# Kernel optimization log

Hardware: AMD Instinct MI355X
Metric: run time of the kernel (lower is better)

Reference implementation:

```python
import jax, jax.numpy as jnp
import numpy as np

NUM_WIRES = 14
N_LAYERS = 2
BATCH = 256
DIM = 2 ** NUM_WIRES


def setup_inputs() -> dict:
    key = jax.random.key(0)
    k1, k2, k3 = jax.random.split(key, 3)
    s = jax.random.normal(k1, (BATCH, DIM), dtype=jnp.float32)
    # StatePrep requires normalized amplitudes
    s = s / jnp.linalg.norm(s, axis=1, keepdims=True)
    params = jax.random.normal(k2, (N_LAYERS, NUM_WIRES, 3), dtype=jnp.float32)
    head_w = jax.random.normal(k3, (1, NUM_WIRES), dtype=jnp.float32) / np.sqrt(NUM_WIRES)
    head_b = jnp.zeros((1,), dtype=jnp.float32)
    return {"state_batch": s, "params": params, "head_w": head_w, "head_b": head_b}


def _ry(t):
    c = jnp.cos(t / 2).astype(jnp.complex64)
    s = jnp.sin(t / 2).astype(jnp.complex64)
    return jnp.stack([jnp.stack([c, -s]), jnp.stack([s, c])])


def _rz(t):
    tc = t.astype(jnp.complex64)
    e_m = jnp.exp(-0.5j * tc)
    e_p = jnp.exp(0.5j * tc)
    z = jnp.zeros((), jnp.complex64)
    return jnp.stack([jnp.stack([e_m, z]), jnp.stack([z, e_p])])


def _rx(t):
    c = jnp.cos(t / 2).astype(jnp.complex64)
    s = (-1j) * jnp.sin(t / 2).astype(jnp.complex64)
    return jnp.stack([jnp.stack([c, s]), jnp.stack([s, c])])


def _apply_1q(psi, U, wire):
    # psi: (B, 2, 2, ..., 2); contract 2x2 gate on axis wire+1 across the batch
    out = jnp.tensordot(U, psi, axes=([1], [wire + 1]))
    return jnp.moveaxis(out, 0, wire + 1)


def _apply_cnot(psi, control, target):
    # flip target axis where control bit == 1
    shape = [1] * psi.ndim
    shape[control + 1] = 2
    mask = (jnp.arange(2) == 1).reshape(shape)
    return jnp.where(mask, jnp.flip(psi, axis=target + 1), psi)


def _circuit(state_c, params):
    psi = state_c.reshape((BATCH,) + (2,) * NUM_WIRES)
    for layer in range(N_LAYERS):
        for w in range(NUM_WIRES):
            psi = _apply_1q(psi, _ry(params[layer, w, 0]), w)
            psi = _apply_1q(psi, _rz(params[layer, w, 1]), w)
            psi = _apply_cnot(psi, w, (w + 1) % NUM_WIRES)
            psi = _apply_1q(psi, _rx(params[layer, w, 2]), w)
    probs = (psi.real ** 2 + psi.imag ** 2).reshape(BATCH, DIM)
    # <Z_w> = sum over basis states of prob * (+1/-1 depending on bit of wire w)
    basis = jnp.arange(DIM)
    shifts = NUM_WIRES - 1 - jnp.arange(NUM_WIRES)  # wire 0 is the MSB axis
    signs = 1.0 - 2.0 * ((basis[None, :] >> shifts[:, None]) & 1).astype(jnp.float32)
    return probs @ signs.T  # (B, NUM_WIRES)


def reference(state_batch, params, head_w, head_b):
    feats = _circuit(state_batch.astype(jnp.complex64), params)  # (B, NUM_WIRES)
    return feats @ head_w[0] + head_b[0]  # (B,)
```

## Files before the change

kernel.cpp:

```cpp
#include <hip/hip_runtime.h>
#include <math.h>

constexpr int NW = 14;
constexpr int DIM = 1 << NW;
constexpr int BATCH = 256;
constexpr int NT = 512;

__device__ __forceinline__ int swz(int i) { return i ^ ((i >> 5) & 31); }

template<int JW, int JT>
__device__ __forceinline__ void apply_gate(float (&ar)[32], float (&ai)[32],
                                           float cy, float sy, float c1, float s1,
                                           float cx, float sx)
{
    constexpr int BW = 1 << JW, BT = 1 << JT;
    #pragma unroll
    for (int m = 0; m < 8; ++m) {
        int l00 = 0, mm = m;
        #pragma unroll
        for (int j = 0; j < 5; ++j) {
            if (j != JW && j != JT) { l00 |= (mm & 1) << j; mm >>= 1; }
        }
        const int iA = l00, iB = l00 | BW, iC = l00 | BT, iD = l00 | BW | BT;

        float a00r = ar[iA], a00i = ai[iA];
        float a10r = ar[iB], a10i = ai[iB];
        float a01r = ar[iC], a01i = ai[iC];
        float a11r = ar[iD], a11i = ai[iD];

        float v0r = cy * a00r - sy * a10r, v0i = cy * a00i - sy * a10i;
        float v1r = sy * a00r + cy * a10r, v1i = sy * a00i + cy * a10i;
        float u0r = cy * a01r - sy * a11r, u0i = cy * a01i - sy * a11i;
        float u1r = sy * a01r + cy * a11r, u1i = sy * a01i + cy * a11i;

        float b00r = c1 * v0r + s1 * v0i, b00i = c1 * v0i - s1 * v0r;
        float b10r = c1 * v1r - s1 * v1i, b10i = c1 * v1i + s1 * v1r;
        float b01r = c1 * u0r + s1 * u0i, b01i = c1 * u0i - s1 * u0r;
        float b11r = c1 * u1r - s1 * u1i, b11i = c1 * u1i + s1 * u1r;

        float o00r = cx * b00r + sx * b11i, o00i = cx * b00i - sx * b11r;
        float o10r = sx * b00i + cx * b11r, o10i = cx * b11i - sx * b00r;
        float o01r = cx * b01r + sx * b10i, o01i = cx * b01i - sx * b10r;
        float o11r = sx * b01i + cx * b10r, o11i = cx * b10i - sx * b01r;

        ar[iA] = o00r; ai[iA] = o00i;
        ar[iB] = o10r; ai[iB] = o10i;
        ar[iC] = o01r; ai[iC] = o01i;
        ar[iD] = o11r; ai[iD] = o11i;
    }
}

template<int P0, int P1, int P2, int P3, int P4>
__device__ __forceinline__ int base_of(int t)
{
    int base = 0, j = 0;
    #pragma unroll
    for (int p = 0; p < NW; ++p) {
        if (p != P0 && p != P1 && p != P2 && p != P3 && p != P4) {
            base |= ((t >> j) & 1) << p;
            ++j;
        }
    }
    return base;
}

template<int P0, int P1, int P2, int P3, int P4>
__device__ __forceinline__ int off_of(int l)
{
    return ((l & 1) << P0) | (((l >> 1) & 1) << P1) | (((l >> 2) & 1) << P2) |
           (((l >> 3) & 1) << P3) | (((l >> 4) & 1) << P4);
}

template<int P0, int P1, int P2, int P3, int P4>
__device__ __forceinline__ void lds_load(const float* re, const float* im,
                                         float (&ar)[32], float (&ai)[32], int base)
{
    #pragma unroll
    for (int l = 0; l < 32; ++l) {
        int s = swz(base | off_of<P0, P1, P2, P3, P4>(l));
        ar[l] = re[s];
        ai[l] = im[s];
    }
}

template<int P0, int P1, int P2, int P3, int P4>
__device__ __forceinline__ void lds_store(float* re, float* im,
                                          const float (&ar)[32], const float (&ai)[32], int base)
{
    #pragma unroll
    for (int l = 0; l < 32; ++l) {
        int s = swz(base | off_of<P0, P1, P2, P3, P4>(l));
        re[s] = ar[l];
        im[s] = ai[l];
    }
}

__global__ __launch_bounds__(NT, 1) void qsim(const float* __restrict__ state,
                                              const float* __restrict__ params,
                                              const float* __restrict__ head_w,
                                              const float* __restrict__ head_b,
                                              float* __restrict__ out)
{
    __shared__ float re[DIM];
    __shared__ float im[DIM];
    __shared__ float2 csv[NW * 3 * 2];
    __shared__ float partial[NT / 64];

    const int t = threadIdx.x;
    const int b = blockIdx.x;

    float ar[32], ai[32];

    const float* __restrict__ sp = state + (size_t)b * DIM;
    #pragma unroll
    for (int l = 0; l < 32; ++l) {
        ar[l] = sp[(l << 9) | t];
        ai[l] = 0.0f;
    }

    if (t < NW * 3 * 2) {
        float sv, cv;
        sincosf(params[t] * 0.5f, &sv, &cv);
        csv[t] = make_float2(cv, sv);
    }
    __syncthreads();

#define GATE(JW, JT, G) do {                                        \
        float2 vy = csv[(G) * 3 + 0];                               \
        float2 vz = csv[(G) * 3 + 1];                               \
        float2 vx = csv[(G) * 3 + 2];                               \
        apply_gate<JW, JT>(ar, ai, vy.x, vy.y, vz.x, vz.y, vx.x, vx.y); \
    } while (0)

    GATE(4, 3, 0); GATE(3, 2, 1); GATE(2, 1, 2); GATE(1, 0, 3);
    lds_store<9, 10, 11, 12, 13>(re, im, ar, ai, base_of<9, 10, 11, 12, 13>(t));
    __syncthreads();

    {
        const int base = base_of<5, 6, 7, 8, 9>(t);
        lds_load<5, 6, 7, 8, 9>(re, im, ar, ai, base);
        GATE(4, 3, 4); GATE(3, 2, 5); GATE(2, 1, 6); GATE(1, 0, 7);
        lds_store<5, 6, 7, 8, 9>(re, im, ar, ai, base);
    }
    __syncthreads();

    {
        const int base = base_of<1, 2, 3, 4, 5>(t);
        lds_load<1, 2, 3, 4, 5>(re, im, ar, ai, base);
        GATE(4, 3, 8); GATE(3, 2, 9); GATE(2, 1, 10); GATE(1, 0, 11);
        lds_store<1, 2, 3, 4, 5>(re, im, ar, ai, base);
    }
    __syncthreads();

    {
        const int base = base_of<0, 1, 11, 12, 13>(t);
        lds_load<0, 1, 11, 12, 13>(re, im, ar, ai, base);
        GATE(1, 0, 12); GATE(0, 4, 13); GATE(4, 3, 14); GATE(3, 2, 15);
        lds_store<0, 1, 11, 12, 13>(re, im, ar, ai, base);
    }
    __syncthreads();

    {
        const int base = base_of<7, 8, 9, 10, 11>(t);
        lds_load<7, 8, 9, 10, 11>(re, im, ar, ai, base);
        GATE(4, 3, 16); GATE(3, 2, 17); GATE(2, 1, 18); GATE(1, 0, 19);
        lds_store<7, 8, 9, 10, 11>(re, im, ar, ai, base);
    }
    __syncthreads();

    {
        const int base = base_of<3, 4, 5, 6, 7>(t);
        lds_load<3, 4, 5, 6, 7>(re, im, ar, ai, base);
        GATE(4, 3, 20); GATE(3, 2, 21); GATE(2, 1, 22); GATE(1, 0, 23);
        lds_store<3, 4, 5, 6, 7>(re, im, ar, ai, base);
    }
    __syncthreads();

    {
        const int base = base_of<0, 1, 2, 3, 13>(t);
        lds_load<0, 1, 2, 3, 13>(re, im, ar, ai, base);
        GATE(3, 2, 24); GATE(2, 1, 25); GATE(1, 0, 26); GATE(0, 4, 27);
    }

    float hw[NW];
    #pragma unroll
    for (int w = 0; w < NW; ++w) hw[w] = head_w[w];

    float gbase = 0.0f;
    #pragma unroll
    for (int j = 0; j < 9; ++j) {
        float h = hw[9 - j];
        gbase += ((t >> j) & 1) ? -h : h;
    }

    float acc = 0.0f;
    #pragma unroll
    for (int l = 0; l < 32; ++l) {
        float g = gbase;
        g += (l & 1)  ? -hw[13] : hw[13];
        g += (l & 2)  ? -hw[12] : hw[12];
        g += (l & 4)  ? -hw[11] : hw[11];
        g += (l & 8)  ? -hw[10] : hw[10];
        g += (l & 16) ? -hw[0]  : hw[0];
        float p = ar[l] * ar[l] + ai[l] * ai[l];
        acc += p * g;
    }

    #pragma unroll
    for (int off = 32; off > 0; off >>= 1) acc += __shfl_down(acc, off);
    if ((t & 63) == 0) partial[t >> 6] = acc;
    __syncthreads();
    if (t == 0) {
        float tot = 0.0f;
        #pragma unroll
        for (int k = 0; k < NT / 64; ++k) tot += partial[k];
        out[b] = tot + head_b[0];
    }
#undef GATE
}

extern "C" void kernel_launch(void* const* d_in, const int* in_sizes, int n_in,
                              void* d_out, int out_size, void* d_ws, size_t ws_size,
                              hipStream_t stream) {
    const float* state  = (const float*)d_in[0];
    const float* params = (const float*)d_in[1];
    const float* head_w = (const float*)d_in[2];
    const float* head_b = (const float*)d_in[3];
    float* outp = (float*)d_out;
    qsim<<<BATCH, NT, 0, stream>>>(state, params, head_w, head_b, outp);
}
```

Baseline: 36.60 us.

## Pack amplitude pairs into float2 vectors for packed-FP32 gate math

Each thread's 32 local amplitudes are regrouped as 16 two-wide vectors, with one qubit axis mapped onto the vector lane, so gate arithmetic can use packed FP32 instructions (v_pk_fma). The qubit-to-slot mapping for every LDS stage changes. Gates acting on the lane qubit use a lane swap in a separate gate routine. This roughly halves ALU instruction count for the gate math, at the cost of lane shuffles and a more complex index mapping.

Result: no change. 36.31 us (-0.8%).

```diff
diff --git a/kernel.cpp b/kernel.cpp
--- a/kernel.cpp
+++ b/kernel.cpp
@@ -1,5 +1,7 @@
 #include <hip/hip_runtime.h>
 #include <math.h>
+
+typedef float v2f __attribute__((ext_vector_type(2)));
 
 constexpr int NW = 14;
 constexpr int DIM = 1 << NW;
@@ -9,44 +11,69 @@
 __device__ __forceinline__ int swz(int i) { return i ^ ((i >> 5) & 31); }
 
 template<int JW, int JT>
-__device__ __forceinline__ void apply_gate(float (&ar)[32], float (&ai)[32],
-                                           float cy, float sy, float c1, float s1,
-                                           float cx, float sx)
+__device__ __forceinline__ void gate_u(v2f (&pr)[16], v2f (&pi)[16],
+                                       float cy, float sy, float c1, float s1,
+                                       float cx, float sx)
 {
     constexpr int BW = 1 << JW, BT = 1 << JT;
     #pragma unroll
-    for (int m = 0; m < 8; ++m) {
+    for (int m = 0; m < 4; ++m) {
         int l00 = 0, mm = m;
         #pragma unroll
-        for (int j = 0; j < 5; ++j) {
+        for (int j = 0; j < 4; ++j)
             if (j != JW && j != JT) { l00 |= (mm & 1) << j; mm >>= 1; }
-        }
         const int iA = l00, iB = l00 | BW, iC = l00 | BT, iD = l00 | BW | BT;
 
-        float a00r = ar[iA], a00i = ai[iA];
-        float a10r = ar[iB], a10i = ai[iB];
-        float a01r = ar[iC], a01i = ai[iC];
-        float a11r = ar[iD], a11i = ai[iD];
-
-        float v0r = cy * a00r - sy * a10r, v0i = cy * a00i - sy * a10i;
-        float v1r = sy * a00r + cy * a10r, v1i = sy * a00i + cy * a10i;
-        float u0r = cy * a01r - sy * a11r, u0i = cy * a01i - sy * a11i;
-        float u1r = sy * a01r + cy * a11r, u1i = sy * a01i + cy * a11i;
-
-        float b00r = c1 * v0r + s1 * v0i, b00i = c1 * v0i - s1 * v0r;
-        float b10r = c1 * v1r - s1 * v1i, b10i = c1 * v1i + s1 * v1r;
-        float b01r = c1 * u0r + s1 * u0i, b01i = c1 * u0i - s1 * u0r;
-        float b11r = c1 * u1r - s1 * u1i, b11i = c1 * u1i + s1 * u1r;
-
-        float o00r = cx * b00r + sx * b11i, o00i = cx * b00i - sx * b11r;
-        float o10r = sx * b00i + cx * b11r, o10i = cx * b11i - sx * b00r;
-        float o01r = cx * b01r + sx * b10i, o01i = cx * b01i - sx * b10r;
-        float o11r = sx * b01i + cx * b10r, o11i = cx * b10i - sx * b01r;
-
-        ar[iA] = o00r; ai[iA] = o00i;
-        ar[iB] = o10r; ai[iB] = o10i;
-        ar[iC] = o01r; ai[iC] = o01i;
-        ar[iD] = o11r; ai[iD] = o11i;
+        v2f a00r = pr[iA], a00i = pi[iA];
+        v2f a10r = pr[iB], a10i = pi[iB];
+        v2f a01r = pr[iC], a01i = pi[iC];
+        v2f a11r = pr[iD], a11i = pi[iD];
+
+        v2f v0r = cy*a00r - sy*a10r, v0i = cy*a00i - sy*a10i;
+        v2f v1r = sy*a00r + cy*a10r, v1i = sy*a00i + cy*a10i;
+        v2f u0r = cy*a01r - sy*a11r, u0i = cy*a01i - sy*a11i;
+        v2f u1r = sy*a01r + cy*a11r, u1i = sy*a01i + cy*a11i;
+
+        v2f b00r = c1*v0r + s1*v0i, b00i = c1*v0i - s1*v0r;
+        v2f b10r = c1*v1r - s1*v1i, b10i = c1*v1i + s1*v1r;
+        v2f b01r = c1*u0r + s1*u0i, b01i = c1*u0i - s1*u0r;
+        v2f b11r = c1*u1r - s1*u1i, b11i = c1*u1i + s1*u1r;
+
+        v2f o00r = cx*b00r + sx*b11i, o00i = cx*b00i - sx*b11r;
+        v2f o10r = sx*b00i + cx*b11r, o10i = cx*b11i - sx*b00r;
+        v2f o01r = cx*b01r + sx*b10i, o01i = cx*b01i - sx*b10r;
+        v2f o11r = sx*b01i + cx*b10r, o11i = cx*b10i - sx*b01r;
+
+        pr[iA] = o00r; pi[iA] = o00i;
+        pr[iB] = o10r; pi[iB] = o10i;
+        pr[iC] = o01r; pi[iC] = o01i;
+        pr[iD] = o11r; pi[iD] = o11i;
+    }
+}
+
+__device__ __forceinline__ void gate_c(v2f (&pr)[16], v2f (&pi)[16],
+                                       float cy, float sy, float c1, float s1,
+                                       float cx, float sx)
+{
+    #pragma unroll
+    for (int m = 0; m < 8; ++m) {
+        const int iA = m << 1, iB = iA | 1;
+        v2f Ar = pr[iA], Ai = pi[iA];
+        v2f Br = pr[iB], Bi = pi[iB];
+
+        v2f Vr = cy*Ar - sy*Br, Vi = cy*Ai - sy*Bi;
+        v2f Wr = sy*Ar + cy*Br, Wi = sy*Ai + cy*Bi;
+
+        v2f P0r = c1*Vr + s1*Vi, P0i = c1*Vi - s1*Vr;
+        v2f P1r = c1*Wr - s1*Wi, P1i = c1*Wi + s1*Wr;
+
+        v2f sP1r = {P1r.y, P1r.x};
+        v2f sP1i = {P1i.y, P1i.x};
+
+        pr[iA] = cx*P0r + sx*sP1i;
+        pi[iA] = cx*P0i - sx*sP1r;
+        pr[iB] = sx*P0i + cx*sP1r;
+        pi[iB] = cx*sP1i - sx*P0r;
     }
 }
 
@@ -72,26 +99,28 @@
 }
 
 template<int P0, int P1, int P2, int P3, int P4>
-__device__ __forceinline__ void lds_load(const float* re, const float* im,
-                                         float (&ar)[32], float (&ai)[32], int base)
-{
-    #pragma unroll
-    for (int l = 0; l < 32; ++l) {
-        int s = swz(base | off_of<P0, P1, P2, P3, P4>(l));
-        ar[l] = re[s];
-        ai[l] = im[s];
-    }
-}
-
-template<int P0, int P1, int P2, int P3, int P4>
-__device__ __forceinline__ void lds_store(float* re, float* im,
-                                          const float (&ar)[32], const float (&ai)[32], int base)
-{
-    #pragma unroll
-    for (int l = 0; l < 32; ++l) {
-        int s = swz(base | off_of<P0, P1, P2, P3, P4>(l));
-        re[s] = ar[l];
-        im[s] = ai[l];
+__device__ __forceinline__ void lds_load_pk(const float* re, const float* im,
+                                            v2f (&pr)[16], v2f (&pi)[16], int base)
+{
+    #pragma unroll
+    for (int k = 0; k < 16; ++k) {
+        const int s0 = swz(base | off_of<P0, P1, P2, P3, P4>(k));
+        const int s1_ = swz(base | off_of<P0, P1, P2, P3, P4>(k | 16));
+        pr[k] = v2f{re[s0], re[s1_]};
+        pi[k] = v2f{im[s0], im[s1_]};
+    }
+}
+
+template<int P0, int P1, int P2, int P3, int P4>
+__device__ __forceinline__ void lds_store_pk(float* re, float* im,
+                                             const v2f (&pr)[16], const v2f (&pi)[16], int base)
+{
+    #pragma unroll
+    for (int k = 0; k < 16; ++k) {
+        const int s0 = swz(base | off_of<P0, P1, P2, P3, P4>(k));
+        const int s1_ = swz(base | off_of<P0, P1, P2, P3, P4>(k | 16));
+        re[s0] = pr[k].x; re[s1_] = pr[k].y;
+        im[s0] = pi[k].x; im[s1_] = pi[k].y;
     }
 }
 
@@ -109,13 +138,13 @@
     const int t = threadIdx.x;
     const int b = blockIdx.x;
 
-    float ar[32], ai[32];
+    v2f pr[16], pi[16];
 
     const float* __restrict__ sp = state + (size_t)b * DIM;
     #pragma unroll
-    for (int l = 0; l < 32; ++l) {
-        ar[l] = sp[(l << 9) | t];
-        ai[l] = 0.0f;
+    for (int k = 0; k < 16; ++k) {
+        pr[k] = v2f{sp[t | (k << 10)], sp[t | (k << 10) | 512]};
+        pi[k] = v2f{0.0f, 0.0f};
     }
 
     if (t < NW * 3 * 2) {
@@ -125,61 +154,68 @@
     }
     __syncthreads();
 
-#define GATE(JW, JT, G) do {                                        \
-        float2 vy = csv[(G) * 3 + 0];                               \
-        float2 vz = csv[(G) * 3 + 1];                               \
-        float2 vx = csv[(G) * 3 + 2];                               \
-        apply_gate<JW, JT>(ar, ai, vy.x, vy.y, vz.x, vz.y, vx.x, vx.y); \
+#define GATEU(JW, JT, G) do {                                           \
+        float2 vy = csv[(G) * 3 + 0];                                   \
+        float2 vz = csv[(G) * 3 + 1];                                   \
+        float2 vx = csv[(G) * 3 + 2];                                   \
+        gate_u<JW, JT>(pr, pi, vy.x, vy.y, vz.x, vz.y, vx.x, vx.y);     \
     } while (0)
-
-    GATE(4, 3, 0); GATE(3, 2, 1); GATE(2, 1, 2); GATE(1, 0, 3);
-    lds_store<9, 10, 11, 12, 13>(re, im, ar, ai, base_of<9, 10, 11, 12, 13>(t));
-    __syncthreads();
-
-    {
-        const int base = base_of<5, 6, 7, 8, 9>(t);
-        lds_load<5, 6, 7, 8, 9>(re, im, ar, ai, base);
-        GATE(4, 3, 4); GATE(3, 2, 5); GATE(2, 1, 6); GATE(1, 0, 7);
-        lds_store<5, 6, 7, 8, 9>(re, im, ar, ai, base);
-    }
-    __syncthreads();
-
-    {
-        const int base = base_of<1, 2, 3, 4, 5>(t);
-        lds_load<1, 2, 3, 4, 5>(re, im, ar, ai, base);
-        GATE(4, 3, 8); GATE(3, 2, 9); GATE(2, 1, 10); GATE(1, 0, 11);
-        lds_store<1, 2, 3, 4, 5>(re, im, ar, ai, base);
-    }
-    __syncthreads();
-
-    {
-        const int base = base_of<0, 1, 11, 12, 13>(t);
-        lds_load<0, 1, 11, 12, 13>(re, im, ar, ai, base);
-        GATE(1, 0, 12); GATE(0, 4, 13); GATE(4, 3, 14); GATE(3, 2, 15);
-        lds_store<0, 1, 11, 12, 13>(re, im, ar, ai, base);
-    }
-    __syncthreads();
-
-    {
-        const int base = base_of<7, 8, 9, 10, 11>(t);
-        lds_load<7, 8, 9, 10, 11>(re, im, ar, ai, base);
-        GATE(4, 3, 16); GATE(3, 2, 17); GATE(2, 1, 18); GATE(1, 0, 19);
-        lds_store<7, 8, 9, 10, 11>(re, im, ar, ai, base);
-    }
-    __syncthreads();
-
-    {
-        const int base = base_of<3, 4, 5, 6, 7>(t);
-        lds_load<3, 4, 5, 6, 7>(re, im, ar, ai, base);
-        GATE(4, 3, 20); GATE(3, 2, 21); GATE(2, 1, 22); GATE(1, 0, 23);
-        lds_store<3, 4, 5, 6, 7>(re, im, ar, ai, base);
+#define GATEC(G) do {                                                   \
+        float2 vy = csv[(G) * 3 + 0];                                   \
+        float2 vz = csv[(G) * 3 + 1];                                   \
+        float2 vx = csv[(G) * 3 + 2];                                   \
+        gate_c(pr, pi, vy.x, vy.y, vz.x, vz.y, vx.x, vx.y);             \
+    } while (0)
+
+
+    GATEU(3, 2, 0); GATEU(2, 1, 1); GATEU(1, 0, 2); GATEC(3);
+    lds_store_pk<10, 11, 12, 13, 9>(re, im, pr, pi, base_of<10, 11, 12, 13, 9>(t));
+    __syncthreads();
+
+    {
+        const int base = base_of<6, 7, 8, 9, 5>(t);
+        lds_load_pk<6, 7, 8, 9, 5>(re, im, pr, pi, base);
+        GATEU(3, 2, 4); GATEU(2, 1, 5); GATEU(1, 0, 6); GATEC(7);
+        lds_store_pk<6, 7, 8, 9, 5>(re, im, pr, pi, base);
+    }
+    __syncthreads();
+
+    {
+        const int base = base_of<2, 3, 4, 5, 1>(t);
+        lds_load_pk<2, 3, 4, 5, 1>(re, im, pr, pi, base);
+        GATEU(3, 2, 8); GATEU(2, 1, 9); GATEU(1, 0, 10); GATEC(11);
+        lds_store_pk<2, 3, 4, 5, 1>(re, im, pr, pi, base);
+    }
+    __syncthreads();
+
+    {
+        const int base = base_of<12, 13, 0, 1, 11>(t);
+        lds_load_pk<12, 13, 0, 1, 11>(re, im, pr, pi, base);
+        GATEU(3, 2, 12); GATEU(2, 1, 13); GATEU(1, 0, 14); GATEC(15);
+        lds_store_pk<12, 13, 0, 1, 11>(re, im, pr, pi, base);
+    }
+    __syncthreads();
+
+    {
+        const int base = base_of<8, 9, 10, 11, 7>(t);
+        lds_load_pk<8, 9, 10, 11, 7>(re, im, pr, pi, base);
+        GATEU(3, 2, 16); GATEU(2, 1, 17); GATEU(1, 0, 18); GATEC(19);
+        lds_store_pk<8, 9, 10, 11, 7>(re, im, pr, pi, base);
+    }
+    __syncthreads();
+
+    {
+        const int base = base_of<4, 5, 6, 7, 3>(t);
+        lds_load_pk<4, 5, 6, 7, 3>(re, im, pr, pi, base);
+        GATEU(3, 2, 20); GATEU(2, 1, 21); GATEU(1, 0, 22); GATEC(23);
+        lds_store_pk<4, 5, 6, 7, 3>(re, im, pr, pi, base);
     }
     __syncthreads();
 
     {
         const int base = base_of<0, 1, 2, 3, 13>(t);
-        lds_load<0, 1, 2, 3, 13>(re, im, ar, ai, base);
-        GATE(3, 2, 24); GATE(2, 1, 25); GATE(1, 0, 26); GATE(0, 4, 27);
+        lds_load_pk<0, 1, 2, 3, 13>(re, im, pr, pi, base);
+        GATEU(3, 2, 24); GATEU(2, 1, 25); GATEU(1, 0, 26); GATEC(27);
     }
 
     float hw[NW];
@@ -193,18 +229,18 @@
         gbase += ((t >> j) & 1) ? -h : h;
     }
 
-    float acc = 0.0f;
-    #pragma unroll
-    for (int l = 0; l < 32; ++l) {
-        float g = gbase;
-        g += (l & 1)  ? -hw[13] : hw[13];
-        g += (l & 2)  ? -hw[12] : hw[12];
-        g += (l & 4)  ? -hw[11] : hw[11];
-        g += (l & 8)  ? -hw[10] : hw[10];
-        g += (l & 16) ? -hw[0]  : hw[0];
-        float p = ar[l] * ar[l] + ai[l] * ai[l];
-        acc += p * g;
-    }
+    v2f acc2 = {0.0f, 0.0f};
+    #pragma unroll
+    for (int k = 0; k < 16; ++k) {
+        float gk = gbase;
+        gk += (k & 1) ? -hw[13] : hw[13];
+        gk += (k & 2) ? -hw[12] : hw[12];
+        gk += (k & 4) ? -hw[11] : hw[11];
+        gk += (k & 8) ? -hw[10] : hw[10];
+        v2f g = {gk + hw[0], gk - hw[0]};
+        acc2 += (pr[k] * pr[k] + pi[k] * pi[k]) * g;
+    }
+    float acc = acc2.x + acc2.y;
 
     #pragma unroll
     for (int off = 32; off > 0; off >>= 1) acc += __shfl_down(acc, off);
@@ -216,7 +252,8 @@
         for (int k = 0; k < NT / 64; ++k) tot += partial[k];
         out[b] = tot + head_b[0];
     }
-#undef GATE
+#undef GATEU
+#undef GATEC
 }
 
 extern "C" void kernel_launch(void* const* d_in, const int* in_sizes, int n_in,
```

## Pack complex amplitudes as float2 with packed-FP32 gate math and new swizzle

Applied to the files above, without the earlier changes.

Stores the statevector in shared memory as interleaved complex float2 instead of separate real/imag arrays, so each amplitude moves with one 64-bit LDS access. A new XOR swizzle is designed for 8-byte accesses, and the register-to-qubit mapping is permuted so gates act on register bits (3,2),(2,1),(1,0),(0,4). Gate arithmetic uses inline v_pk_mul_f32/v_pk_fma_f32 with op_sel/neg modifiers to process real and imaginary parts together, roughly halving VALU instruction count. The risks are correctness of the hand-written op_sel encodings and the bank-conflict behaviour of the new swizzle.

Measured after the change: 36.50 us. About the same (-0.3%).

```diff
diff --git a/kernel.cpp b/kernel.cpp
--- a/kernel.cpp
+++ b/kernel.cpp
@@ -1,52 +1,69 @@
 #include <hip/hip_runtime.h>
 #include <math.h>
+
+typedef float v2f __attribute__((ext_vector_type(2)));
 
 constexpr int NW = 14;
 constexpr int DIM = 1 << NW;
 constexpr int BATCH = 256;
 constexpr int NT = 512;
 
-__device__ __forceinline__ int swz(int i) { return i ^ ((i >> 5) & 31); }
+__device__ __host__ constexpr int swz2(int i) {
+    return i ^ ((i >> 4) & 15)
+             ^ (((i >> 8) & 7) << 1)
+             ^ ((i >> 11) & 1)
+             ^ (((i >> 12) & 3) << 1);
+}
+
+__device__ __forceinline__ v2f pkmul_lo(v2f P, v2f B) {
+    v2f d; asm("v_pk_mul_f32 %0, %1, %2 op_sel:[0,0] op_sel_hi:[0,1]"
+               : "=v"(d) : "v"(P), "v"(B)); return d;
+}
+__device__ __forceinline__ v2f pkfma_hi(v2f P, v2f B, v2f C) {
+    v2f d; asm("v_pk_fma_f32 %0, %1, %2, %3 op_sel:[1,0,0] op_sel_hi:[1,1,1]"
+               : "=v"(d) : "v"(P), "v"(B), "v"(C)); return d;
+}
+__device__ __forceinline__ v2f pkfmn_hi(v2f P, v2f B, v2f C) {
+    v2f d; asm("v_pk_fma_f32 %0, %1, %2, %3 op_sel:[1,0,0] op_sel_hi:[1,1,1] neg_lo:[1,0,0] neg_hi:[1,0,0]"
+               : "=v"(d) : "v"(P), "v"(B), "v"(C)); return d;
+}
+__device__ __forceinline__ v2f cfma_p(v2f P, v2f B, v2f C) {
+    v2f d; asm("v_pk_fma_f32 %0, %1, %2, %3 op_sel:[1,1,0] op_sel_hi:[1,0,1] neg_hi:[0,1,0]"
+               : "=v"(d) : "v"(P), "v"(B), "v"(C)); return d;
+}
+__device__ __forceinline__ v2f cfma_m(v2f P, v2f B, v2f C) {
+    v2f d; asm("v_pk_fma_f32 %0, %1, %2, %3 op_sel:[1,1,0] op_sel_hi:[1,0,1] neg_lo:[0,1,0]"
+               : "=v"(d) : "v"(P), "v"(B), "v"(C)); return d;
+}
 
 template<int JW, int JT>
-__device__ __forceinline__ void apply_gate(float (&ar)[32], float (&ai)[32],
-                                           float cy, float sy, float c1, float s1,
-                                           float cx, float sx)
+__device__ __forceinline__ void gate_u(v2f (&a)[32], v2f Y, v2f Z, v2f X)
 {
     constexpr int BW = 1 << JW, BT = 1 << JT;
     #pragma unroll
     for (int m = 0; m < 8; ++m) {
         int l00 = 0, mm = m;
         #pragma unroll
-        for (int j = 0; j < 5; ++j) {
+        for (int j = 0; j < 5; ++j)
             if (j != JW && j != JT) { l00 |= (mm & 1) << j; mm >>= 1; }
-        }
         const int iA = l00, iB = l00 | BW, iC = l00 | BT, iD = l00 | BW | BT;
 
-        float a00r = ar[iA], a00i = ai[iA];
-        float a10r = ar[iB], a10i = ai[iB];
-        float a01r = ar[iC], a01i = ai[iC];
-        float a11r = ar[iD], a11i = ai[iD];
-
-        float v0r = cy * a00r - sy * a10r, v0i = cy * a00i - sy * a10i;
-        float v1r = sy * a00r + cy * a10r, v1i = sy * a00i + cy * a10i;
-        float u0r = cy * a01r - sy * a11r, u0i = cy * a01i - sy * a11i;
-        float u1r = sy * a01r + cy * a11r, u1i = sy * a01i + cy * a11i;
-
-        float b00r = c1 * v0r + s1 * v0i, b00i = c1 * v0i - s1 * v0r;
-        float b10r = c1 * v1r - s1 * v1i, b10i = c1 * v1i + s1 * v1r;
-        float b01r = c1 * u0r + s1 * u0i, b01i = c1 * u0i - s1 * u0r;
-        float b11r = c1 * u1r - s1 * u1i, b11i = c1 * u1i + s1 * u1r;
-
-        float o00r = cx * b00r + sx * b11i, o00i = cx * b00i - sx * b11r;
-        float o10r = sx * b00i + cx * b11r, o10i = cx * b11i - sx * b00r;
-        float o01r = cx * b01r + sx * b10i, o01i = cx * b01i - sx * b10r;
-        float o11r = sx * b01i + cx * b10r, o11i = cx * b10i - sx * b01r;
-
-        ar[iA] = o00r; ai[iA] = o00i;
-        ar[iB] = o10r; ai[iB] = o10i;
-        ar[iC] = o01r; ai[iC] = o01i;
-        ar[iD] = o11r; ai[iD] = o11i;
+        v2f a00 = a[iA], a10 = a[iB], a01 = a[iC], a11 = a[iD];
+
+        v2f v0 = pkfmn_hi(Y, a10, pkmul_lo(Y, a00));
+        v2f v1 = pkfma_hi(Y, a00, pkmul_lo(Y, a10));
+        v2f u0 = pkfmn_hi(Y, a11, pkmul_lo(Y, a01));
+        v2f u1 = pkfma_hi(Y, a01, pkmul_lo(Y, a11));
+
+        v2f b00 = cfma_p(Z, v0, pkmul_lo(Z, v0));
+        v2f b10 = cfma_m(Z, v1, pkmul_lo(Z, v1));
+        v2f b01 = cfma_p(Z, u0, pkmul_lo(Z, u0));
+        v2f b11 = cfma_m(Z, u1, pkmul_lo(Z, u1));
+
+        a[iA] = cfma_p(X, b11, pkmul_lo(X, b00));
+        a[iB] = cfma_p(X, b00, pkmul_lo(X, b11));
+        a[iC] = cfma_p(X, b10, pkmul_lo(X, b01));
+        a[iD] = cfma_p(X, b01, pkmul_lo(X, b10));
     }
 }
 
@@ -72,26 +89,22 @@
 }
 
 template<int P0, int P1, int P2, int P3, int P4>
-__device__ __forceinline__ void lds_load(const float* re, const float* im,
-                                         float (&ar)[32], float (&ai)[32], int base)
-{
-    #pragma unroll
-    for (int l = 0; l < 32; ++l) {
-        int s = swz(base | off_of<P0, P1, P2, P3, P4>(l));
-        ar[l] = re[s];
-        ai[l] = im[s];
-    }
-}
-
-template<int P0, int P1, int P2, int P3, int P4>
-__device__ __forceinline__ void lds_store(float* re, float* im,
-                                          const float (&ar)[32], const float (&ai)[32], int base)
-{
-    #pragma unroll
-    for (int l = 0; l < 32; ++l) {
-        int s = swz(base | off_of<P0, P1, P2, P3, P4>(l));
-        re[s] = ar[l];
-        im[s] = ai[l];
+__device__ __forceinline__ void lds_load(const float2* cs, v2f (&a)[32], int sb)
+{
+    #pragma unroll
+    for (int l = 0; l < 32; ++l) {
+        const int addr = sb ^ swz2(off_of<P0, P1, P2, P3, P4>(l));
+        a[l] = *(const v2f*)(cs + addr);
+    }
+}
+
+template<int P0, int P1, int P2, int P3, int P4>
+__device__ __forceinline__ void lds_store(float2* cs, const v2f (&a)[32], int sb)
+{
+    #pragma unroll
+    for (int l = 0; l < 32; ++l) {
+        const int addr = sb ^ swz2(off_of<P0, P1, P2, P3, P4>(l));
+        *(v2f*)(cs + addr) = a[l];
     }
 }
 
@@ -101,21 +114,19 @@
                                               const float* __restrict__ head_b,
                                               float* __restrict__ out)
 {
-    __shared__ float re[DIM];
-    __shared__ float im[DIM];
+    __shared__ float2 cs[DIM];
     __shared__ float2 csv[NW * 3 * 2];
     __shared__ float partial[NT / 64];
 
     const int t = threadIdx.x;
     const int b = blockIdx.x;
 
-    float ar[32], ai[32];
+    v2f a[32];
 
     const float* __restrict__ sp = state + (size_t)b * DIM;
     #pragma unroll
     for (int l = 0; l < 32; ++l) {
-        ar[l] = sp[(l << 9) | t];
-        ai[l] = 0.0f;
+        a[l] = v2f{sp[t | off_of<10, 11, 12, 13, 9>(l)], 0.0f};
     }
 
     if (t < NW * 3 * 2) {
@@ -125,61 +136,62 @@
     }
     __syncthreads();
 
-#define GATE(JW, JT, G) do {                                        \
-        float2 vy = csv[(G) * 3 + 0];                               \
-        float2 vz = csv[(G) * 3 + 1];                               \
-        float2 vx = csv[(G) * 3 + 2];                               \
-        apply_gate<JW, JT>(ar, ai, vy.x, vy.y, vz.x, vz.y, vx.x, vx.y); \
+#define GU(JW, JT, G) do {                                              \
+        v2f Y = *(const v2f*)&csv[(G) * 3 + 0];                         \
+        v2f Z = *(const v2f*)&csv[(G) * 3 + 1];                         \
+        v2f X = *(const v2f*)&csv[(G) * 3 + 2];                         \
+        gate_u<JW, JT>(a, Y, Z, X);                                     \
     } while (0)
 
-    GATE(4, 3, 0); GATE(3, 2, 1); GATE(2, 1, 2); GATE(1, 0, 3);
-    lds_store<9, 10, 11, 12, 13>(re, im, ar, ai, base_of<9, 10, 11, 12, 13>(t));
-    __syncthreads();
-
-    {
-        const int base = base_of<5, 6, 7, 8, 9>(t);
-        lds_load<5, 6, 7, 8, 9>(re, im, ar, ai, base);
-        GATE(4, 3, 4); GATE(3, 2, 5); GATE(2, 1, 6); GATE(1, 0, 7);
-        lds_store<5, 6, 7, 8, 9>(re, im, ar, ai, base);
-    }
-    __syncthreads();
-
-    {
-        const int base = base_of<1, 2, 3, 4, 5>(t);
-        lds_load<1, 2, 3, 4, 5>(re, im, ar, ai, base);
-        GATE(4, 3, 8); GATE(3, 2, 9); GATE(2, 1, 10); GATE(1, 0, 11);
-        lds_store<1, 2, 3, 4, 5>(re, im, ar, ai, base);
-    }
-    __syncthreads();
-
-    {
-        const int base = base_of<0, 1, 11, 12, 13>(t);
-        lds_load<0, 1, 11, 12, 13>(re, im, ar, ai, base);
-        GATE(1, 0, 12); GATE(0, 4, 13); GATE(4, 3, 14); GATE(3, 2, 15);
-        lds_store<0, 1, 11, 12, 13>(re, im, ar, ai, base);
-    }
-    __syncthreads();
-
-    {
-        const int base = base_of<7, 8, 9, 10, 11>(t);
-        lds_load<7, 8, 9, 10, 11>(re, im, ar, ai, base);
-        GATE(4, 3, 16); GATE(3, 2, 17); GATE(2, 1, 18); GATE(1, 0, 19);
-        lds_store<7, 8, 9, 10, 11>(re, im, ar, ai, base);
-    }
-    __syncthreads();
-
-    {
-        const int base = base_of<3, 4, 5, 6, 7>(t);
-        lds_load<3, 4, 5, 6, 7>(re, im, ar, ai, base);
-        GATE(4, 3, 20); GATE(3, 2, 21); GATE(2, 1, 22); GATE(1, 0, 23);
-        lds_store<3, 4, 5, 6, 7>(re, im, ar, ai, base);
-    }
-    __syncthreads();
-
-    {
-        const int base = base_of<0, 1, 2, 3, 13>(t);
-        lds_load<0, 1, 2, 3, 13>(re, im, ar, ai, base);
-        GATE(3, 2, 24); GATE(2, 1, 25); GATE(1, 0, 26); GATE(0, 4, 27);
+
+    GU(3, 2, 0); GU(2, 1, 1); GU(1, 0, 2); GU(0, 4, 3);
+    lds_store<10, 11, 12, 13, 9>(cs, a, swz2(base_of<10, 11, 12, 13, 9>(t)));
+    __syncthreads();
+
+    {
+        const int sb = swz2(base_of<6, 7, 8, 9, 5>(t));
+        lds_load<6, 7, 8, 9, 5>(cs, a, sb);
+        GU(3, 2, 4); GU(2, 1, 5); GU(1, 0, 6); GU(0, 4, 7);
+        lds_store<6, 7, 8, 9, 5>(cs, a, sb);
+    }
+    __syncthreads();
+
+    {
+        const int sb = swz2(base_of<2, 3, 4, 5, 1>(t));
+        lds_load<2, 3, 4, 5, 1>(cs, a, sb);
+        GU(3, 2, 8); GU(2, 1, 9); GU(1, 0, 10); GU(0, 4, 11);
+        lds_store<2, 3, 4, 5, 1>(cs, a, sb);
+    }
+    __syncthreads();
+
+    {
+        const int sb = swz2(base_of<12, 13, 0, 1, 11>(t));
+        lds_load<12, 13, 0, 1, 11>(cs, a, sb);
+        GU(3, 2, 12); GU(2, 1, 13); GU(1, 0, 14); GU(0, 4, 15);
+        lds_store<12, 13, 0, 1, 11>(cs, a, sb);
+    }
+    __syncthreads();
+
+    {
+        const int sb = swz2(base_of<8, 9, 10, 11, 7>(t));
+        lds_load<8, 9, 10, 11, 7>(cs, a, sb);
+        GU(3, 2, 16); GU(2, 1, 17); GU(1, 0, 18); GU(0, 4, 19);
+        lds_store<8, 9, 10, 11, 7>(cs, a, sb);
+    }
+    __syncthreads();
+
+    {
+        const int sb = swz2(base_of<4, 5, 6, 7, 3>(t));
+        lds_load<4, 5, 6, 7, 3>(cs, a, sb);
+        GU(3, 2, 20); GU(2, 1, 21); GU(1, 0, 22); GU(0, 4, 23);
+        lds_store<4, 5, 6, 7, 3>(cs, a, sb);
+    }
+    __syncthreads();
+
+    {
+        const int sb = swz2(base_of<0, 1, 2, 3, 13>(t));
+        lds_load<0, 1, 2, 3, 13>(cs, a, sb);
+        GU(3, 2, 24); GU(2, 1, 25); GU(1, 0, 26); GU(0, 4, 27);
     }
 
     float hw[NW];
@@ -202,8 +214,7 @@
         g += (l & 4)  ? -hw[11] : hw[11];
         g += (l & 8)  ? -hw[10] : hw[10];
         g += (l & 16) ? -hw[0]  : hw[0];
-        float p = ar[l] * ar[l] + ai[l] * ai[l];
-        acc += p * g;
+        acc += (a[l].x * a[l].x + a[l].y * a[l].y) * g;
     }
 
     #pragma unroll
@@ -216,7 +227,7 @@
         for (int k = 0; k < NT / 64; ++k) tot += partial[k];
         out[b] = tot + head_b[0];
     }
-#undef GATE
+#undef GU
 }
 
 extern "C" void kernel_launch(void* const* d_in, const int* in_sizes, int n_in,
```
